# Kernel tuning notes

Measured on AMD Instinct MI355X. Metric: run time of the kernel, lower is better.

## Reference

```python
import jax, jax.numpy as jnp
import numpy as np

N_NODES = 50000
N_EDGES = 800000
D_FEAT = 64
N_OUT = 64
N_LAYERS = 2


def setup_inputs() -> dict:
    key = jax.random.key(0)
    ks = jax.random.split(key, 6)
    x = jax.random.normal(ks[0], (N_NODES, D_FEAT), dtype=jnp.float32)
    rows = jnp.sort(jax.random.randint(ks[1], (N_EDGES,), 0, N_NODES, dtype=jnp.int32))
    cols = jax.random.randint(ks[2], (N_EDGES,), 0, N_NODES, dtype=jnp.int32)
    vals = jax.random.uniform(ks[3], (N_EDGES,), dtype=jnp.float32)
    scalars = jnp.ones((N_LAYERS,), dtype=jnp.float32)  # per-layer scalar param (init ones)
    W = jax.random.normal(ks[4], (N_OUT, D_FEAT), dtype=jnp.float32) / np.sqrt(D_FEAT)
    b = jnp.zeros((N_OUT,), dtype=jnp.float32)
    return {"x": x, "rows": rows, "cols": cols, "vals": vals,
            "scalars": scalars, "W": W, "b": b}


def _spmm(rows, cols, vals, x):
    # y[r] = sum_e vals[e] * x[cols[e]]  (sparse adj in COO)
    msgs = vals[:, None] * x[cols]  # [E, D] gather + scale
    return jax.ops.segment_sum(msgs, rows, num_segments=N_NODES,
                               indices_are_sorted=True)


def reference(x, rows, cols, vals, scalars, W, b):
    # ScalarGCNNoFeatureTrans forward (dropout in eval mode = identity)
    h = x
    for l in range(N_LAYERS):
        h = jax.nn.elu(_spmm(rows, cols, vals, scalars[l] * h))
    return h @ W.T + b
```

## Files before the change

kernel.cpp:

```cpp
#include <hip/hip_runtime.h>
#include <hip/hip_fp16.h>
#include <math.h>

#define N_NODES 50000
#define N_EDGES 800000
#define D_FEAT 64
#define XCHUNKS (N_NODES * D_FEAT / 8)
#define NBLK 3125

__device__ __forceinline__ unsigned pack2h(float a, float b) {
    __half2 h = __floats2half2_rn(a, b);
    return *reinterpret_cast<unsigned*>(&h);
}
__device__ __forceinline__ __half2 as_h2(unsigned u) {
    return *reinterpret_cast<__half2*>(&u);
}

__device__ __forceinline__ float elu_f(float x) {
    return x > 0.f ? x : (__expf(x) - 1.f);
}

__global__ __launch_bounds__(256) void prep_kernel(const int* __restrict__ rows,
                                                   const int* __restrict__ cols,
                                                   const float* __restrict__ vals,
                                                   const float* __restrict__ x,
                                                   int* __restrict__ row_ptr,
                                                   int2* __restrict__ pairs,
                                                   unsigned short* __restrict__ xhf,
                                                   int do_pack) {
    const int i = blockIdx.x * blockDim.x + threadIdx.x;
    if (i <= N_NODES) {
        int lo = 0, hi = N_EDGES;
        while (lo < hi) {
            int mid = (lo + hi) >> 1;
            if (rows[mid] < i) lo = mid + 1; else hi = mid;
        }
        row_ptr[i] = lo;
    }
    if (do_pack && i < N_EDGES) {
        const float v = vals[i];
        pairs[i] = make_int2(cols[i] << 7, (int)pack2h(v, v));
    }
    if (i < XCHUNKS) {
        const float4 f0 = *reinterpret_cast<const float4*>(x + (size_t)i * 8);
        const float4 f1 = *reinterpret_cast<const float4*>(x + (size_t)i * 8 + 4);
        uint4 w;
        w.x = pack2h(f0.x, f0.y);
        w.y = pack2h(f0.z, f0.w);
        w.z = pack2h(f1.x, f1.y);
        w.w = pack2h(f1.z, f1.w);
        *reinterpret_cast<uint4*>(xhf + (size_t)i * 8) = w;
    }
}

template <bool PACKED, bool MASKED>
__device__ __forceinline__ void edge_step8(const char* __restrict__ hb,
                                           const int2* __restrict__ pairs,
                                           const int* __restrict__ cols,
                                           const float* __restrict__ vals,
                                           int e, int e1, int boff,
                                           __half2& A0, __half2& A1,
                                           __half2& B0, __half2& B1) {
    int off[8]; unsigned v2[8];
    #pragma unroll
    for (int k = 0; k < 8; ++k) {
        const int t = e + k;
        const int idx = MASKED ? (t < e1 ? t : e1 - 1) : t;
        if constexpr (PACKED) {
            const int2 p = pairs[idx];
            off[k] = p.x;
            v2[k]  = (unsigned)p.y;
        } else {
            off[k] = cols[idx] << 7;
            const float v = vals[idx];
            v2[k] = pack2h(v, v);
        }
        if (MASKED) v2[k] = (t < e1) ? v2[k] : 0u;
    }
    uint2 gg[8];
    #pragma unroll
    for (int k = 0; k < 8; ++k)
        gg[k] = *reinterpret_cast<const uint2*>(hb + (unsigned)(off[k] + boff));
    #pragma unroll
    for (int k = 0; k < 8; ++k) {
        const __half2 vv = as_h2(v2[k]);
        if (k & 1) {
            B0 = __hfma2(vv, as_h2(gg[k].x), B0);
            B1 = __hfma2(vv, as_h2(gg[k].y), B1);
        } else {
            A0 = __hfma2(vv, as_h2(gg[k].x), A0);
            A1 = __hfma2(vv, as_h2(gg[k].y), A1);
        }
    }
}

template <bool FUSE, bool PACKED>
__global__ __launch_bounds__(256) void gcn_layer(
    const unsigned short* __restrict__ h_in,
    const int2*  __restrict__ pairs,
    const int*   __restrict__ cols,
    const float* __restrict__ vals,
    const int*   __restrict__ row_ptr,
    const float* __restrict__ scalar_p,
    const float* __restrict__ W,
    const float* __restrict__ bvec,
    void*        __restrict__ h_out)
{
    __shared__ float Wlds[FUSE ? 64 * 65 : 1];
    __shared__ float ylds[FUSE ? 4 * 4 * 68 : 1];

    const int lane = threadIdx.x & 63;
    const int wave = threadIdx.x >> 6;
    const int g    = lane >> 4;
    const int f4   = lane & 15;
    const int boff = f4 * 8;

    if constexpr (FUSE) {
        for (int i = threadIdx.x; i < 64 * 64; i += 256)
            Wlds[(i >> 6) * 65 + (i & 63)] = W[i];
        __syncthreads();
    }

    const int row = blockIdx.x * 16 + wave * 4 + g;
    const float s  = scalar_p[0];
    const int  e0  = row_ptr[row];
    const int  e1  = row_ptr[row + 1];
    const char* hb = (const char*)h_in;

    __half2 A0 = __floats2half2_rn(0.f, 0.f);
    __half2 A1 = A0, B0 = A0, B1 = A0;

    int e = e0;
    for (; e + 8 <= e1; e += 8)
        edge_step8<PACKED, false>(hb, pairs, cols, vals, e, e1, boff, A0, A1, B0, B1);
    if (e < e1)
        edge_step8<PACKED, true>(hb, pairs, cols, vals, e, e1, boff, A0, A1, B0, B1);

    const float2 a0 = __half22float2(A0), a1 = __half22float2(A1);
    const float2 b0 = __half22float2(B0), b1 = __half22float2(B1);
    float4 acc;
    acc.x = elu_f((a0.x + b0.x) * s);
    acc.y = elu_f((a0.y + b0.y) * s);
    acc.z = elu_f((a1.x + b1.x) * s);
    acc.w = elu_f((a1.y + b1.y) * s);

    if constexpr (!FUSE) {
        uint2 wv;
        wv.x = pack2h(acc.x, acc.y);
        wv.y = pack2h(acc.z, acc.w);
        *reinterpret_cast<uint2*>((char*)h_out + (size_t)row * 128 + boff) = wv;
    } else {
        float* yw = ylds + wave * (4 * 68);
        *reinterpret_cast<float4*>(yw + g * 68 + f4 * 4) = acc;
        asm volatile("s_waitcnt lgkmcnt(0)" ::: "memory");

        const int j = lane;
        const float bj = bvec[j];
        float o0 = bj, o1 = bj, o2 = bj, o3 = bj;
        #pragma unroll
        for (int d0 = 0; d0 < 16; ++d0) {
            const float* wr = Wlds + j * 65 + d0 * 4;
            const float w0 = wr[0], w1 = wr[1], w2 = wr[2], w3 = wr[3];
            const float4 y0 = *reinterpret_cast<const float4*>(yw + 0 * 68 + d0 * 4);
            const float4 y1 = *reinterpret_cast<const float4*>(yw + 1 * 68 + d0 * 4);
            const float4 y2 = *reinterpret_cast<const float4*>(yw + 2 * 68 + d0 * 4);
            const float4 y3 = *reinterpret_cast<const float4*>(yw + 3 * 68 + d0 * 4);
            o0 = fmaf(y0.x, w0, o0); o0 = fmaf(y0.y, w1, o0);
            o0 = fmaf(y0.z, w2, o0); o0 = fmaf(y0.w, w3, o0);
            o1 = fmaf(y1.x, w0, o1); o1 = fmaf(y1.y, w1, o1);
            o1 = fmaf(y1.z, w2, o1); o1 = fmaf(y1.w, w3, o1);
            o2 = fmaf(y2.x, w0, o2); o2 = fmaf(y2.y, w1, o2);
            o2 = fmaf(y2.z, w2, o2); o2 = fmaf(y2.w, w3, o2);
            o3 = fmaf(y3.x, w0, o3); o3 = fmaf(y3.y, w1, o3);
            o3 = fmaf(y3.z, w2, o3); o3 = fmaf(y3.w, w3, o3);
        }
        const size_t rbase = (size_t)(blockIdx.x * 16 + wave * 4) * D_FEAT;
        float* outp = (float*)h_out;
        outp[rbase + 0 * D_FEAT + j] = o0;
        outp[rbase + 1 * D_FEAT + j] = o1;
        outp[rbase + 2 * D_FEAT + j] = o2;
        outp[rbase + 3 * D_FEAT + j] = o3;
    }
}

extern "C" void kernel_launch(void* const* d_in, const int* in_sizes, int n_in,
                              void* d_out, int out_size, void* d_ws, size_t ws_size,
                              hipStream_t stream) {
    const float* x       = (const float*)d_in[0];
    const int*   rows    = (const int*)  d_in[1];
    const int*   cols    = (const int*)  d_in[2];
    const float* vals    = (const float*)d_in[3];
    const float* scalars = (const float*)d_in[4];
    const float* W       = (const float*)d_in[5];
    const float* b       = (const float*)d_in[6];
    float* out = (float*)d_out;

    const size_t rp_b = (sizeof(int) * (N_NODES + 1) + 255) & ~size_t(255);
    const size_t xb_b = ((size_t)N_NODES * D_FEAT * 2 + 255) & ~size_t(255);
    const size_t pr_b = sizeof(int2) * (size_t)N_EDGES;

    int*            row_ptr = (int*)d_ws;
    unsigned short* xhf     = (unsigned short*)((char*)d_ws + rp_b);
    unsigned short* h1      = (unsigned short*)((char*)d_ws + rp_b + xb_b);
    const bool packed = ws_size >= rp_b + 2 * xb_b + pr_b;
    int2* pairs = packed ? (int2*)((char*)d_ws + rp_b + 2 * xb_b) : nullptr;

    prep_kernel<<<(N_EDGES + 255) / 256, 256, 0, stream>>>(
        rows, cols, vals, x, row_ptr, pairs, xhf, packed ? 1 : 0);

    if (packed) {
        gcn_layer<false, true><<<NBLK, 256, 0, stream>>>(
            xhf, pairs, cols, vals, row_ptr, scalars + 0, nullptr, nullptr, h1);
        gcn_layer<true, true><<<NBLK, 256, 0, stream>>>(
            h1, pairs, cols, vals, row_ptr, scalars + 1, W, b, out);
    } else {
        gcn_layer<false, false><<<NBLK, 256, 0, stream>>>(
            xhf, nullptr, cols, vals, row_ptr, scalars + 0, nullptr, nullptr, h1);
        gcn_layer<true, false><<<NBLK, 256, 0, stream>>>(
            h1, nullptr, cols, vals, row_ptr, scalars + 1, W, b, out);
    }
}
```

Measured before the change: 58.32 us.

## Stage per-block edge lists in LDS and drop the global packed-pairs buffer

Each block now cooperatively loads its 16 rows' cols/vals (up to 512 edges) into shared memory as packed offset/half2-value pairs, replacing the prep pass that wrote a global pairs array. Edges beyond the cap fall back to a scalar global loop. The fused layer also stores W as packed halves in LDS, and the prep grid shrinks to cover only the x conversion. This removes the 6.4 MB pairs write and the read-back of pairs twice, at the cost of redundant cols/vals reads in both layers, an extra barrier, and slightly lower W precision.

```diff
diff --git a/kernel.cpp b/kernel.cpp
--- a/kernel.cpp
+++ b/kernel.cpp
@@ -7,6 +7,7 @@
 #define D_FEAT 64
 #define XCHUNKS (N_NODES * D_FEAT / 8)
 #define NBLK 3125
+#define ECAP 512
 
 __device__ __forceinline__ unsigned pack2h(float a, float b) {
     __half2 h = __floats2half2_rn(a, b);
@@ -21,13 +22,9 @@
 }
 
 __global__ __launch_bounds__(256) void prep_kernel(const int* __restrict__ rows,
-                                                   const int* __restrict__ cols,
-                                                   const float* __restrict__ vals,
                                                    const float* __restrict__ x,
                                                    int* __restrict__ row_ptr,
-                                                   int2* __restrict__ pairs,
-                                                   unsigned short* __restrict__ xhf,
-                                                   int do_pack) {
+                                                   unsigned short* __restrict__ xhf) {
     const int i = blockIdx.x * blockDim.x + threadIdx.x;
     if (i <= N_NODES) {
         int lo = 0, hi = N_EDGES;
@@ -36,10 +33,6 @@
             if (rows[mid] < i) lo = mid + 1; else hi = mid;
         }
         row_ptr[i] = lo;
-    }
-    if (do_pack && i < N_EDGES) {
-        const float v = vals[i];
-        pairs[i] = make_int2(cols[i] << 7, (int)pack2h(v, v));
     }
     if (i < XCHUNKS) {
         const float4 f0 = *reinterpret_cast<const float4*>(x + (size_t)i * 8);
@@ -53,29 +46,21 @@
     }
 }
 
-template <bool PACKED, bool MASKED>
-__device__ __forceinline__ void edge_step8(const char* __restrict__ hb,
-                                           const int2* __restrict__ pairs,
-                                           const int* __restrict__ cols,
-                                           const float* __restrict__ vals,
-                                           int e, int e1, int boff,
-                                           __half2& A0, __half2& A1,
-                                           __half2& B0, __half2& B1) {
+template <bool MASKED>
+__device__ __forceinline__ void edge_step8_lds(const char* __restrict__ hb,
+                                               const int2* __restrict__ elds,
+                                               int le, int le1, int boff,
+                                               __half2& A0, __half2& A1,
+                                               __half2& B0, __half2& B1) {
     int off[8]; unsigned v2[8];
     #pragma unroll
     for (int k = 0; k < 8; ++k) {
-        const int t = e + k;
-        const int idx = MASKED ? (t < e1 ? t : e1 - 1) : t;
-        if constexpr (PACKED) {
-            const int2 p = pairs[idx];
-            off[k] = p.x;
-            v2[k]  = (unsigned)p.y;
-        } else {
-            off[k] = cols[idx] << 7;
-            const float v = vals[idx];
-            v2[k] = pack2h(v, v);
-        }
-        if (MASKED) v2[k] = (t < e1) ? v2[k] : 0u;
+        const int t = le + k;
+        const int idx = MASKED ? (t < le1 ? t : le1 - 1) : t;
+        const int2 p = elds[idx];
+        off[k] = p.x;
+        v2[k]  = (unsigned)p.y;
+        if (MASKED) v2[k] = (t < le1) ? v2[k] : 0u;
     }
     uint2 gg[8];
     #pragma unroll
@@ -94,10 +79,9 @@
     }
 }
 
-template <bool FUSE, bool PACKED>
+template <bool FUSE>
 __global__ __launch_bounds__(256) void gcn_layer(
     const unsigned short* __restrict__ h_in,
-    const int2*  __restrict__ pairs,
     const int*   __restrict__ cols,
     const float* __restrict__ vals,
     const int*   __restrict__ row_ptr,
@@ -106,22 +90,35 @@
     const float* __restrict__ bvec,
     void*        __restrict__ h_out)
 {
-    __shared__ float Wlds[FUSE ? 64 * 65 : 1];
-    __shared__ float ylds[FUSE ? 4 * 4 * 68 : 1];
-
-    const int lane = threadIdx.x & 63;
-    const int wave = threadIdx.x >> 6;
+    __shared__ int2     elds[ECAP];
+    __shared__ unsigned Wh[FUSE ? 64 * 33 : 1];
+    __shared__ float    ylds[FUSE ? 4 * 4 * 68 : 1];
+
+    const int tid  = threadIdx.x;
+    const int lane = tid & 63;
+    const int wave = tid >> 6;
     const int g    = lane >> 4;
     const int f4   = lane & 15;
     const int boff = f4 * 8;
 
+    const int rb  = blockIdx.x * 16;
+    const int eb0 = row_ptr[rb];
+    const int eb1 = row_ptr[rb + 16];
+    const int cnt = min(eb1 - eb0, ECAP);
+    for (int i = tid; i < cnt; i += 256) {
+        const int   c = cols[eb0 + i];
+        const float v = vals[eb0 + i];
+        elds[i] = make_int2(c << 7, (int)pack2h(v, v));
+    }
     if constexpr (FUSE) {
-        for (int i = threadIdx.x; i < 64 * 64; i += 256)
-            Wlds[(i >> 6) * 65 + (i & 63)] = W[i];
-        __syncthreads();
-    }
-
-    const int row = blockIdx.x * 16 + wave * 4 + g;
+        for (int i = tid; i < 64 * 32; i += 256) {
+            const int j = i >> 5, c = i & 31;
+            Wh[j * 33 + c] = pack2h(W[j * 64 + 2 * c], W[j * 64 + 2 * c + 1]);
+        }
+    }
+    __syncthreads();
+
+    const int row = rb + wave * 4 + g;
     const float s  = scalar_p[0];
     const int  e0  = row_ptr[row];
     const int  e1  = row_ptr[row + 1];
@@ -130,11 +127,22 @@
     __half2 A0 = __floats2half2_rn(0.f, 0.f);
     __half2 A1 = A0, B0 = A0, B1 = A0;
 
-    int e = e0;
-    for (; e + 8 <= e1; e += 8)
-        edge_step8<PACKED, false>(hb, pairs, cols, vals, e, e1, boff, A0, A1, B0, B1);
-    if (e < e1)
-        edge_step8<PACKED, true>(hb, pairs, cols, vals, e, e1, boff, A0, A1, B0, B1);
+    const int ecap = eb0 + cnt;
+    const int le0 = e0 - eb0;
+    const int le1 = (e1 < ecap ? e1 : ecap) - eb0;
+    int le = le0;
+    for (; le + 8 <= le1; le += 8)
+        edge_step8_lds<false>(hb, elds, le, le1, boff, A0, A1, B0, B1);
+    if (le < le1)
+        edge_step8_lds<true>(hb, elds, le, le1, boff, A0, A1, B0, B1);
+    for (int e = (e0 > ecap ? e0 : ecap); e < e1; ++e) {
+        const int   c = cols[e];
+        const float v = vals[e];
+        const __half2 vv = as_h2(pack2h(v, v));
+        const uint2 gg = *reinterpret_cast<const uint2*>(hb + (unsigned)((c << 7) + boff));
+        A0 = __hfma2(vv, as_h2(gg.x), A0);
+        A1 = __hfma2(vv, as_h2(gg.y), A1);
+    }
 
     const float2 a0 = __half22float2(A0), a1 = __half22float2(A1);
     const float2 b0 = __half22float2(B0), b1 = __half22float2(B1);
@@ -159,22 +167,22 @@
         float o0 = bj, o1 = bj, o2 = bj, o3 = bj;
         #pragma unroll
         for (int d0 = 0; d0 < 16; ++d0) {
-            const float* wr = Wlds + j * 65 + d0 * 4;
-            const float w0 = wr[0], w1 = wr[1], w2 = wr[2], w3 = wr[3];
+            const float2 wA = __half22float2(as_h2(Wh[j * 33 + 2 * d0]));
+            const float2 wB = __half22float2(as_h2(Wh[j * 33 + 2 * d0 + 1]));
             const float4 y0 = *reinterpret_cast<const float4*>(yw + 0 * 68 + d0 * 4);
             const float4 y1 = *reinterpret_cast<const float4*>(yw + 1 * 68 + d0 * 4);
             const float4 y2 = *reinterpret_cast<const float4*>(yw + 2 * 68 + d0 * 4);
             const float4 y3 = *reinterpret_cast<const float4*>(yw + 3 * 68 + d0 * 4);
-            o0 = fmaf(y0.x, w0, o0); o0 = fmaf(y0.y, w1, o0);
-            o0 = fmaf(y0.z, w2, o0); o0 = fmaf(y0.w, w3, o0);
-            o1 = fmaf(y1.x, w0, o1); o1 = fmaf(y1.y, w1, o1);
-            o1 = fmaf(y1.z, w2, o1); o1 = fmaf(y1.w, w3, o1);
-            o2 = fmaf(y2.x, w0, o2); o2 = fmaf(y2.y, w1, o2);
-            o2 = fmaf(y2.z, w2, o2); o2 = fmaf(y2.w, w3, o2);
-            o3 = fmaf(y3.x, w0, o3); o3 = fmaf(y3.y, w1, o3);
-            o3 = fmaf(y3.z, w2, o3); o3 = fmaf(y3.w, w3, o3);
-        }
-        const size_t rbase = (size_t)(blockIdx.x * 16 + wave * 4) * D_FEAT;
+            o0 = fmaf(y0.x, wA.x, o0); o0 = fmaf(y0.y, wA.y, o0);
+            o0 = fmaf(y0.z, wB.x, o0); o0 = fmaf(y0.w, wB.y, o0);
+            o1 = fmaf(y1.x, wA.x, o1); o1 = fmaf(y1.y, wA.y, o1);
+            o1 = fmaf(y1.z, wB.x, o1); o1 = fmaf(y1.w, wB.y, o1);
+            o2 = fmaf(y2.x, wA.x, o2); o2 = fmaf(y2.y, wA.y, o2);
+            o2 = fmaf(y2.z, wB.x, o2); o2 = fmaf(y2.w, wB.y, o2);
+            o3 = fmaf(y3.x, wA.x, o3); o3 = fmaf(y3.y, wA.y, o3);
+            o3 = fmaf(y3.z, wB.x, o3); o3 = fmaf(y3.w, wB.y, o3);
+        }
+        const size_t rbase = (size_t)(rb + wave * 4) * D_FEAT;
         float* outp = (float*)h_out;
         outp[rbase + 0 * D_FEAT + j] = o0;
         outp[rbase + 1 * D_FEAT + j] = o1;
@@ -197,26 +205,15 @@
 
     const size_t rp_b = (sizeof(int) * (N_NODES + 1) + 255) & ~size_t(255);
     const size_t xb_b = ((size_t)N_NODES * D_FEAT * 2 + 255) & ~size_t(255);
-    const size_t pr_b = sizeof(int2) * (size_t)N_EDGES;
 
     int*            row_ptr = (int*)d_ws;
     unsigned short* xhf     = (unsigned short*)((char*)d_ws + rp_b);
     unsigned short* h1      = (unsigned short*)((char*)d_ws + rp_b + xb_b);
-    const bool packed = ws_size >= rp_b + 2 * xb_b + pr_b;
-    int2* pairs = packed ? (int2*)((char*)d_ws + rp_b + 2 * xb_b) : nullptr;
-
-    prep_kernel<<<(N_EDGES + 255) / 256, 256, 0, stream>>>(
-        rows, cols, vals, x, row_ptr, pairs, xhf, packed ? 1 : 0);
-
-    if (packed) {
-        gcn_layer<false, true><<<NBLK, 256, 0, stream>>>(
-            xhf, pairs, cols, vals, row_ptr, scalars + 0, nullptr, nullptr, h1);
-        gcn_layer<true, true><<<NBLK, 256, 0, stream>>>(
-            h1, pairs, cols, vals, row_ptr, scalars + 1, W, b, out);
-    } else {
-        gcn_layer<false, false><<<NBLK, 256, 0, stream>>>(
-            xhf, nullptr, cols, vals, row_ptr, scalars + 0, nullptr, nullptr, h1);
-        gcn_layer<true, false><<<NBLK, 256, 0, stream>>>(
-            h1, nullptr, cols, vals, row_ptr, scalars + 1, W, b, out);
-    }
-}
+
+    prep_kernel<<<(XCHUNKS + 255) / 256, 256, 0, stream>>>(rows, x, row_ptr, xhf);
+
+    gcn_layer<false><<<NBLK, 256, 0, stream>>>(
+        xhf, cols, vals, row_ptr, scalars + 0, nullptr, nullptr, h1);
+    gcn_layer<true><<<NBLK, 256, 0, stream>>>(
+        h1, cols, vals, row_ptr, scalars + 1, W, b, out);
+}
```

Measured after the change: 48.88 us, median of 2. 1.19x faster.
